# Performance work log

Measured on AMD Instinct MI355X. Metric: run time of the kernel, lower is better.

## Reference

```python
import jax, jax.numpy as jnp
import numpy as np

EMBED_LEN = 512
NUM_FEA = 8   # M
NUM_CLS = 14  # C
BETA = 0.3
BATCH = 8192


def setup_inputs() -> dict:
    key = jax.random.key(0)
    k1, k2, k3 = jax.random.split(key, 3)
    x = jax.random.normal(k1, (BATCH, EMBED_LEN * NUM_FEA), dtype=jnp.float32)
    wordvec_array = jax.random.normal(k2, (1, EMBED_LEN, NUM_CLS), dtype=jnp.float32)
    y = jax.random.randint(k3, (BATCH, NUM_CLS), 0, 2, dtype=jnp.int32)
    # guarantee at least one positive and one negative label per sample
    y = y.at[:, 0].set(1).at[:, -1].set(0)
    return {"x": x, "y": y, "wordvec_array": wordvec_array}


def reference(x, y, wordvec_array):
    B = x.shape[0]
    un = x.reshape(B, EMBED_LEN, -1)            # [B, E, M]
    w = wordvec_array[0]                         # [E, C]
    # dot_prod_all[b, c] = max_m <un[b,:,m], w[:,c]>
    dot = jnp.einsum('bem,ec->bmc', un, w).max(axis=1)   # [B, C]

    P = (y == 1).astype(x.dtype)                 # positive mask [B, C]
    N = 1.0 - P                                  # negative mask [B, C]
    npos = P.sum(axis=-1)                        # [B]
    nneg = N.sum(axis=-1)                        # [B]

    # pairwise v[b,p,n] = dot_neg - dot_pos; sum softplus over masked pairs
    V = dot[:, None, :] - dot[:, :, None]        # [B, C(pos), C(neg)]
    pair_sum = jnp.einsum('bp,bn,bpn->b', P, N, jax.nn.softplus(V))
    # edge case: no negatives -> v = -dot_pos
    noneg_sum = jnp.sum(P * jax.nn.softplus(-dot), axis=-1)
    S = jnp.where(nneg > 0, pair_sum, noneg_sum)
    base = S / npos                              # [B]

    # diversity: unbiased variance of positive-class word vectors over class dim
    mean_w = jnp.einsum('bc,ec->be', P, w) / npos[:, None]          # [B, E]
    ss = jnp.einsum('bc,bec->be', P, (w[None] - mean_w[:, :, None]) ** 2)
    var_w = ss / jnp.maximum(npos - 1.0, 1.0)[:, None]
    var_w = jnp.where((npos == 1.0)[:, None], 0.0, var_w)           # sig = 0 if single positive
    total_var = var_w.sum(axis=-1)               # [B]

    # var_regularization: unbiased var over M, L1 over embed dim
    sig2 = jnp.var(un, axis=2, ddof=1)           # [B, E]
    l1_err = jnp.abs(sig2).sum(axis=-1)          # [B]

    # num_fea > 1 branch
    loss = 2.0 * ((1.0 - BETA) * (1.0 + total_var) * base + BETA * l1_err)
    return loss.mean()
```

## Files before the change

kernel.cpp:

```cpp
#include <hip/hip_runtime.h>
#include <math.h>

#define E_LEN 512
#define M_FEA 8
#define C_CLS 14
#define BATCH 8192
#define S_PER_BLOCK 4

template<int CTRL>
__device__ __forceinline__ float dpp_mov_f(float v) {
  return __int_as_float(__builtin_amdgcn_update_dpp(
      0, __float_as_int(v), CTRL, 0xF, 0xF, false));
}
__device__ __forceinline__ float sum16(float v) {
  v += dpp_mov_f<0x128>(v);
  v += dpp_mov_f<0x124>(v);
  v += dpp_mov_f<0x122>(v);
  v += dpp_mov_f<0x121>(v);
  return v;
}
__device__ __forceinline__ float sum4_16(float v) {
  v += dpp_mov_f<0x128>(v);
  v += dpp_mov_f<0x124>(v);
  return v;
}
__device__ __forceinline__ float max8(float v) {
  v = fmaxf(v, dpp_mov_f<0xB1>(v));
  v = fmaxf(v, dpp_mov_f<0x4E>(v));
  v = fmaxf(v, dpp_mov_f<0x141>(v));
  return v;
}
__device__ __forceinline__ float softplus_f(float v) {
  return fmaxf(v, 0.f) + __logf(1.f + __expf(-fabsf(v)));
}

__global__ void MID_LOSS_prep(const float* __restrict__ w,
                              float* __restrict__ wsf,
                              float* __restrict__ out) {
  __shared__ float wc[E_LEN];
  __shared__ float red[16];
  const int tid = threadIdx.x;
  const int c = blockIdx.x;

  for (int i = tid; i < E_LEN; i += 256) wc[i] = w[i * C_CLS + c];
  __syncthreads();

  const int h = (c >= 7) ? 1 : 0;
  const int ci = c - h * 7;
  for (int i = tid; i < E_LEN; i += 256) {
    int pos = (ci < 6) ? (h * 3584 + (ci >> 1) * 1024 + 2 * i + (ci & 1))
                       : (h * 3584 + 3072 + i);
    wsf[pos] = wc[i];
  }

  for (int c2 = 0; c2 < C_CLS; ++c2) {
    float part = 0.f;
    for (int i = tid; i < E_LEN; i += 256) part = fmaf(wc[i], w[i * C_CLS + c2], part);
    part = sum16(part);
    if ((tid & 15) == 0) red[tid >> 4] = part;
    __syncthreads();
    if (tid == 0) {
      float s = 0.f;
      for (int r = 0; r < 16; ++r) s += red[r];
      wsf[7168 + c * C_CLS + c2] = s;
    }
    __syncthreads();
  }
  if (c == 0 && tid == 0) out[0] = 0.f;
}

__global__ __launch_bounds__(256, 3)
void MID_LOSS_main(const float* __restrict__ x, const int* __restrict__ y,
                   const float* __restrict__ wsf, float* __restrict__ out) {
  __shared__ float w_lds[7168];
  __shared__ float G_lds[196];
  __shared__ float P_lds[C_CLS];
  __shared__ float dotc_lds[C_CLS];
  __shared__ float scratch[14 * 264];
  __shared__ float pair_scr[16];
  __shared__ float g_scr[16];
  __shared__ float l1_scr[8];

  const int tid = threadIdx.x;
  const int lane = tid & 63;
  const int wid = tid >> 6;
  const int ch = wid & 1;
  const int eh = wid >> 1;

#pragma unroll
  for (int i = 0; i < 7; ++i) {
    int idx = tid + i * 256;
    ((float4*)w_lds)[idx] = ((const float4*)wsf)[idx];
  }
  if (tid < 196) G_lds[tid] = wsf[7168 + tid];

  float block_loss = 0.f;

  for (int s = 0; s < S_PER_BLOCK; ++s) {
    const int b = blockIdx.x * S_PER_BLOCK + s;
    const float* xrow = x + (size_t)b * (E_LEN * M_FEA);

    __syncthreads();
    if (tid < C_CLS) P_lds[tid] = (y[b * C_CLS + tid] == 1) ? 1.f : 0.f;

    float U[4][8];
#pragma unroll
    for (int j = 0; j < 4; ++j) {
      const int e = eh * 256 + j * 64 + lane;
      *(float4*)&U[j][0] = *(const float4*)(xrow + e * 8);
      *(float4*)&U[j][4] = *(const float4*)(xrow + e * 8 + 4);
    }
    float acc[7][8];
#pragma unroll
    for (int ci = 0; ci < 7; ++ci)
#pragma unroll
      for (int m = 0; m < 8; ++m) acc[ci][m] = 0.f;
    float l1 = 0.f;
    const float* wb = w_lds + ch * 3584;
#pragma unroll
    for (int j = 0; j < 4; ++j) {
      const int e = eh * 256 + j * 64 + lane;
#pragma unroll
      for (int cp = 0; cp < 3; ++cp) {
        const float2 w2 = *(const float2*)(wb + cp * 1024 + 2 * e);
#pragma unroll
        for (int m = 0; m < 8; ++m) {
          acc[2 * cp][m]     = fmaf(U[j][m], w2.x, acc[2 * cp][m]);
          acc[2 * cp + 1][m] = fmaf(U[j][m], w2.y, acc[2 * cp + 1][m]);
        }
      }
      const float w1 = wb[3072 + e];
#pragma unroll
      for (int m = 0; m < 8; ++m) acc[6][m] = fmaf(U[j][m], w1, acc[6][m]);

      if (ch == 0) {
        float s1 = 0.f, s2 = 0.f;
#pragma unroll
        for (int m = 0; m < 8; ++m) {
          s1 += U[j][m];
          s2 = fmaf(U[j][m], U[j][m], s2);
        }
        const float sig = (s2 - s1 * s1 * 0.125f) * (1.f / 7.f);
        l1 += fabsf(sig);
      }
    }
#pragma unroll
    for (int ci = 0; ci < 7; ++ci)
#pragma unroll
      for (int m = 0; m < 8; ++m) acc[ci][m] = sum4_16(acc[ci][m]);
    if ((lane & 15) < 4) {
      const int part = eh * 16 + (lane >> 4) * 4 + (lane & 3);
#pragma unroll
      for (int ci = 0; ci < 7; ++ci) {
        const int c = ch * 7 + ci;
        *(float4*)(scratch + c * 264 + part * 8) =
            make_float4(acc[ci][0], acc[ci][1], acc[ci][2], acc[ci][3]);
        *(float4*)(scratch + c * 264 + part * 8 + 4) =
            make_float4(acc[ci][4], acc[ci][5], acc[ci][6], acc[ci][7]);
      }
    }
    if (ch == 0) {
      const float l1s = sum16(l1);
      if ((lane & 15) == 0) l1_scr[eh * 4 + (lane >> 4)] = l1s;
    }
    __syncthreads();

    if (wid < 2) {
      const int craw = tid >> 3;
      const int c = (craw > 13) ? 13 : craw;
      const int m = tid & 7;
      float dv = 0.f;
#pragma unroll
      for (int p = 0; p < 32; ++p) dv += scratch[c * 264 + p * 8 + m];
      dv = max8(dv);
      if ((tid & 7) == 0 && craw < 14) dotc_lds[c] = dv;
    }
    __syncthreads();

    {
      const int tt = (tid < 196) ? tid : 0;
      const int p = tt / 14;
      const int n = tt - p * 14;
      const float act = (tid < 196) ? 1.f : 0.f;
      const float Pp = P_lds[p];
      const float Pn = P_lds[n];
      const float v = dotc_lds[n] - dotc_lds[p];
      float aP = act * Pp * (1.f - Pn) * softplus_f(v);
      float aG = act * Pp * Pn * G_lds[tt];
      aP = sum16(aP);
      aG = sum16(aG);
      if ((lane & 15) == 0) {
        pair_scr[tid >> 4] = aP;
        g_scr[tid >> 4] = aG;
      }
    }
    __syncthreads();

    if (tid == 0) {
      float S = 0.f, sumG = 0.f;
#pragma unroll
      for (int r = 0; r < 16; ++r) { S += pair_scr[r]; sumG += g_scr[r]; }
      float l1e = 0.f;
#pragma unroll
      for (int r = 0; r < 8; ++r) l1e += l1_scr[r];
      float npos = 0.f;
      for (int c = 0; c < C_CLS; ++c) npos += P_lds[c];
      const float nneg = (float)C_CLS - npos;
      float base;
      if (nneg > 0.f) {
        base = S / npos;
      } else {
        float t = 0.f;
        for (int c = 0; c < C_CLS; ++c)
          if (P_lds[c] > 0.5f) t += softplus_f(-dotc_lds[c]);
        base = t / npos;
      }
      float sumW2 = 0.f;
      for (int c = 0; c < C_CLS; ++c) sumW2 += P_lds[c] * G_lds[c * C_CLS + c];
      float tv = 0.f;
      if (npos > 1.5f) tv = (sumW2 - sumG / npos) / (npos - 1.f);
      block_loss += 1.4f * (1.f + tv) * base + 0.6f * l1e;
    }
  }
  if (tid == 0) atomicAdd(out, block_loss * (1.f / (float)BATCH));
}

extern "C" void kernel_launch(void* const* d_in, const int* in_sizes, int n_in,
                              void* d_out, int out_size, void* d_ws, size_t ws_size,
                              hipStream_t stream) {
  const float* x = (const float*)d_in[0];
  const int* y = (const int*)d_in[1];
  const float* w = (const float*)d_in[2];
  float* out = (float*)d_out;
  float* wsf = (float*)d_ws;

  MID_LOSS_prep<<<C_CLS, 256, 0, stream>>>(w, wsf, out);
  MID_LOSS_main<<<BATCH / S_PER_BLOCK, 256, 0, stream>>>(x, y, wsf, out);
}
```

Baseline: 218.4 us.

## Split work across M halves, spread atomics over slots, add final reduction

The main kernel now splits waves by feature half instead of class half, so each thread loads only four features and accumulates all 14 classes, with the variance partials exchanged through LDS. The weight permutation moves from the prep kernel into each main block's load phase. The single global atomic is replaced by 256 slot atomics plus a small finishing kernel. Prep collapses to one block computing the Gram matrix. The aims are less per-thread register pressure, less atomic contention and a balanced L1-variance workload. The cost is an extra kernel launch and per-block index math during the weight load.

```diff
diff --git a/kernel.cpp b/kernel.cpp
--- a/kernel.cpp
+++ b/kernel.cpp
@@ -2,10 +2,10 @@
 #include <math.h>
 
 #define E_LEN 512
-#define M_FEA 8
 #define C_CLS 14
 #define BATCH 8192
 #define S_PER_BLOCK 4
+#define NSLOTS 256
 
 template<int CTRL>
 __device__ __forceinline__ float dpp_mov_f(float v) {
@@ -35,145 +35,144 @@
 }
 
 __global__ void MID_LOSS_prep(const float* __restrict__ w,
-                              float* __restrict__ wsf,
-                              float* __restrict__ out) {
-  __shared__ float wc[E_LEN];
-  __shared__ float red[16];
+                              float* __restrict__ wsf) {
+  __shared__ float wl[E_LEN * C_CLS];
   const int tid = threadIdx.x;
-  const int c = blockIdx.x;
-
-  for (int i = tid; i < E_LEN; i += 256) wc[i] = w[i * C_CLS + c];
+#pragma unroll
+  for (int i = 0; i < 7; ++i)
+    ((float4*)wl)[tid + i * 256] = ((const float4*)w)[tid + i * 256];
+  wsf[tid] = 0.f;
   __syncthreads();
-
-  const int h = (c >= 7) ? 1 : 0;
-  const int ci = c - h * 7;
-  for (int i = tid; i < E_LEN; i += 256) {
-    int pos = (ci < 6) ? (h * 3584 + (ci >> 1) * 1024 + 2 * i + (ci & 1))
-                       : (h * 3584 + 3072 + i);
-    wsf[pos] = wc[i];
+  if (tid < 196) {
+    const int p = tid / 14, n = tid - p * 14;
+    float g = 0.f;
+    for (int e = 0; e < E_LEN; ++e)
+      g = fmaf(wl[e * 14 + p], wl[e * 14 + n], g);
+    wsf[NSLOTS + tid] = g;
   }
-
-  for (int c2 = 0; c2 < C_CLS; ++c2) {
-    float part = 0.f;
-    for (int i = tid; i < E_LEN; i += 256) part = fmaf(wc[i], w[i * C_CLS + c2], part);
-    part = sum16(part);
-    if ((tid & 15) == 0) red[tid >> 4] = part;
-    __syncthreads();
-    if (tid == 0) {
-      float s = 0.f;
-      for (int r = 0; r < 16; ++r) s += red[r];
-      wsf[7168 + c * C_CLS + c2] = s;
-    }
-    __syncthreads();
-  }
-  if (c == 0 && tid == 0) out[0] = 0.f;
 }
 
 __global__ __launch_bounds__(256, 3)
 void MID_LOSS_main(const float* __restrict__ x, const int* __restrict__ y,
-                   const float* __restrict__ wsf, float* __restrict__ out) {
-  __shared__ float w_lds[7168];
-  __shared__ float G_lds[196];
-  __shared__ float P_lds[C_CLS];
-  __shared__ float dotc_lds[C_CLS];
-  __shared__ float scratch[14 * 264];
-  __shared__ float pair_scr[16];
-  __shared__ float g_scr[16];
-  __shared__ float l1_scr[8];
+                   const float* __restrict__ w, const float* __restrict__ wsf,
+                   float* __restrict__ slots) {
+  __shared__ float wp_s[7 * 1024];
+  __shared__ float scr[14 * 264];
+  __shared__ float var_s[E_LEN * 2];
+  __shared__ float G_s[196];
+  __shared__ float P_s[C_CLS];
+  __shared__ float dot_s[C_CLS];
+  __shared__ float pair_scr[16], g_scr[16], l1_scr[8];
 
   const int tid = threadIdx.x;
   const int lane = tid & 63;
   const int wid = tid >> 6;
-  const int ch = wid & 1;
+  const int mh = wid & 1;
   const int eh = wid >> 1;
 
 #pragma unroll
   for (int i = 0; i < 7; ++i) {
-    int idx = tid + i * 256;
-    ((float4*)w_lds)[idx] = ((const float4*)wsf)[idx];
+    const int idx = tid + i * 256;
+    const float4 v = ((const float4*)w)[idx];
+    const float vv[4] = {v.x, v.y, v.z, v.w};
+#pragma unroll
+    for (int k = 0; k < 4; ++k) {
+      const int f = idx * 4 + k;
+      const int e = f / 14;
+      const int c = f - e * 14;
+      wp_s[(c >> 1) * 1024 + e * 2 + (c & 1)] = vv[k];
+    }
   }
-  if (tid < 196) G_lds[tid] = wsf[7168 + tid];
+  if (tid < 196) G_s[tid] = wsf[NSLOTS + tid];
 
   float block_loss = 0.f;
 
   for (int s = 0; s < S_PER_BLOCK; ++s) {
     const int b = blockIdx.x * S_PER_BLOCK + s;
-    const float* xrow = x + (size_t)b * (E_LEN * M_FEA);
-
-    __syncthreads();
-    if (tid < C_CLS) P_lds[tid] = (y[b * C_CLS + tid] == 1) ? 1.f : 0.f;
-
-    float U[4][8];
+    const float* xrow = x + (size_t)b * (E_LEN * 8);
+
+    __syncthreads();
+    if (tid < C_CLS) P_s[tid] = (y[b * C_CLS + tid] == 1) ? 1.f : 0.f;
+
+    float U[4][4];
 #pragma unroll
     for (int j = 0; j < 4; ++j) {
       const int e = eh * 256 + j * 64 + lane;
-      *(float4*)&U[j][0] = *(const float4*)(xrow + e * 8);
-      *(float4*)&U[j][4] = *(const float4*)(xrow + e * 8 + 4);
-    }
-    float acc[7][8];
-#pragma unroll
-    for (int ci = 0; ci < 7; ++ci)
-#pragma unroll
-      for (int m = 0; m < 8; ++m) acc[ci][m] = 0.f;
-    float l1 = 0.f;
-    const float* wb = w_lds + ch * 3584;
+      *(float4*)U[j] = *(const float4*)(xrow + e * 8 + mh * 4);
+    }
+    float vs1[4], vs2[4];
+#pragma unroll
+    for (int j = 0; j < 4; ++j) {
+      float s1 = U[j][0] + U[j][1] + U[j][2] + U[j][3];
+      float s2 = U[j][0] * U[j][0];
+      s2 = fmaf(U[j][1], U[j][1], s2);
+      s2 = fmaf(U[j][2], U[j][2], s2);
+      s2 = fmaf(U[j][3], U[j][3], s2);
+      vs1[j] = s1;
+      vs2[j] = s2;
+    }
+    if (mh == 1) {
+#pragma unroll
+      for (int j = 0; j < 4; ++j) {
+        const int e = eh * 256 + j * 64 + lane;
+        *(float2*)(var_s + e * 2) = make_float2(vs1[j], vs2[j]);
+      }
+    }
+    float acc[14][4];
+#pragma unroll
+    for (int c = 0; c < 14; ++c)
+#pragma unroll
+      for (int m = 0; m < 4; ++m) acc[c][m] = 0.f;
 #pragma unroll
     for (int j = 0; j < 4; ++j) {
       const int e = eh * 256 + j * 64 + lane;
-#pragma unroll
-      for (int cp = 0; cp < 3; ++cp) {
-        const float2 w2 = *(const float2*)(wb + cp * 1024 + 2 * e);
-#pragma unroll
-        for (int m = 0; m < 8; ++m) {
+      const float* wb = wp_s + e * 2;
+#pragma unroll
+      for (int cp = 0; cp < 7; ++cp) {
+        const float2 w2 = *(const float2*)(wb + cp * 1024);
+#pragma unroll
+        for (int m = 0; m < 4; ++m) {
           acc[2 * cp][m]     = fmaf(U[j][m], w2.x, acc[2 * cp][m]);
           acc[2 * cp + 1][m] = fmaf(U[j][m], w2.y, acc[2 * cp + 1][m]);
         }
       }
-      const float w1 = wb[3072 + e];
-#pragma unroll
-      for (int m = 0; m < 8; ++m) acc[6][m] = fmaf(U[j][m], w1, acc[6][m]);
-
-      if (ch == 0) {
-        float s1 = 0.f, s2 = 0.f;
-#pragma unroll
-        for (int m = 0; m < 8; ++m) {
-          s1 += U[j][m];
-          s2 = fmaf(U[j][m], U[j][m], s2);
-        }
+    }
+#pragma unroll
+    for (int c = 0; c < 14; ++c)
+#pragma unroll
+      for (int m = 0; m < 4; ++m) acc[c][m] = sum4_16(acc[c][m]);
+    if ((lane & 15) < 4) {
+      const int part = eh * 16 + (lane >> 4) * 4 + (lane & 3);
+#pragma unroll
+      for (int c = 0; c < 14; ++c)
+        *(float4*)(scr + c * 264 + part * 8 + mh * 4) =
+            make_float4(acc[c][0], acc[c][1], acc[c][2], acc[c][3]);
+    }
+    __syncthreads();
+
+    if (mh == 1) {
+      const int r = eh * 64 + lane;
+      const int craw = r >> 3;
+      const int c = (craw > 13) ? 13 : craw;
+      const int m = r & 7;
+      float dv = 0.f;
+#pragma unroll
+      for (int p = 0; p < 32; ++p) dv += scr[c * 264 + p * 8 + m];
+      dv = max8(dv);
+      if ((r & 7) == 0 && craw < 14) dot_s[c] = dv;
+    } else {
+      float l1 = 0.f;
+#pragma unroll
+      for (int j = 0; j < 4; ++j) {
+        const int e = eh * 256 + j * 64 + lane;
+        const float2 o = *(const float2*)(var_s + e * 2);
+        const float s1 = vs1[j] + o.x;
+        const float s2 = vs2[j] + o.y;
         const float sig = (s2 - s1 * s1 * 0.125f) * (1.f / 7.f);
         l1 += fabsf(sig);
       }
-    }
-#pragma unroll
-    for (int ci = 0; ci < 7; ++ci)
-#pragma unroll
-      for (int m = 0; m < 8; ++m) acc[ci][m] = sum4_16(acc[ci][m]);
-    if ((lane & 15) < 4) {
-      const int part = eh * 16 + (lane >> 4) * 4 + (lane & 3);
-#pragma unroll
-      for (int ci = 0; ci < 7; ++ci) {
-        const int c = ch * 7 + ci;
-        *(float4*)(scratch + c * 264 + part * 8) =
-            make_float4(acc[ci][0], acc[ci][1], acc[ci][2], acc[ci][3]);
-        *(float4*)(scratch + c * 264 + part * 8 + 4) =
-            make_float4(acc[ci][4], acc[ci][5], acc[ci][6], acc[ci][7]);
-      }
-    }
-    if (ch == 0) {
-      const float l1s = sum16(l1);
-      if ((lane & 15) == 0) l1_scr[eh * 4 + (lane >> 4)] = l1s;
-    }
-    __syncthreads();
-
-    if (wid < 2) {
-      const int craw = tid >> 3;
-      const int c = (craw > 13) ? 13 : craw;
-      const int m = tid & 7;
-      float dv = 0.f;
-#pragma unroll
-      for (int p = 0; p < 32; ++p) dv += scratch[c * 264 + p * 8 + m];
-      dv = max8(dv);
-      if ((tid & 7) == 0 && craw < 14) dotc_lds[c] = dv;
+      l1 = sum16(l1);
+      if ((lane & 15) == 0) l1_scr[eh * 4 + (lane >> 4)] = l1;
     }
     __syncthreads();
 
@@ -182,11 +181,11 @@
       const int p = tt / 14;
       const int n = tt - p * 14;
       const float act = (tid < 196) ? 1.f : 0.f;
-      const float Pp = P_lds[p];
-      const float Pn = P_lds[n];
-      const float v = dotc_lds[n] - dotc_lds[p];
+      const float Pp = P_s[p];
+      const float Pn = P_s[n];
+      const float v = dot_s[n] - dot_s[p];
       float aP = act * Pp * (1.f - Pn) * softplus_f(v);
-      float aG = act * Pp * Pn * G_lds[tt];
+      float aG = act * Pp * Pn * G_s[tt];
       aP = sum16(aP);
       aG = sum16(aG);
       if ((lane & 15) == 0) {
@@ -199,30 +198,41 @@
     if (tid == 0) {
       float S = 0.f, sumG = 0.f;
 #pragma unroll
-      for (int r = 0; r < 16; ++r) { S += pair_scr[r]; sumG += g_scr[r]; }
+      for (int r2 = 0; r2 < 16; ++r2) { S += pair_scr[r2]; sumG += g_scr[r2]; }
       float l1e = 0.f;
 #pragma unroll
-      for (int r = 0; r < 8; ++r) l1e += l1_scr[r];
+      for (int r2 = 0; r2 < 8; ++r2) l1e += l1_scr[r2];
       float npos = 0.f;
-      for (int c = 0; c < C_CLS; ++c) npos += P_lds[c];
-      const float nneg = (float)C_CLS - npos;
+      for (int c = 0; c < 14; ++c) npos += P_s[c];
+      const float nneg = 14.f - npos;
       float base;
       if (nneg > 0.f) {
         base = S / npos;
       } else {
-        float t = 0.f;
-        for (int c = 0; c < C_CLS; ++c)
-          if (P_lds[c] > 0.5f) t += softplus_f(-dotc_lds[c]);
-        base = t / npos;
+        float t2 = 0.f;
+        for (int c = 0; c < 14; ++c)
+          if (P_s[c] > 0.5f) t2 += softplus_f(-dot_s[c]);
+        base = t2 / npos;
       }
       float sumW2 = 0.f;
-      for (int c = 0; c < C_CLS; ++c) sumW2 += P_lds[c] * G_lds[c * C_CLS + c];
+      for (int c = 0; c < 14; ++c) sumW2 += P_s[c] * G_s[c * 14 + c];
       float tv = 0.f;
       if (npos > 1.5f) tv = (sumW2 - sumG / npos) / (npos - 1.f);
       block_loss += 1.4f * (1.f + tv) * base + 0.6f * l1e;
     }
   }
-  if (tid == 0) atomicAdd(out, block_loss * (1.f / (float)BATCH));
+  if (tid == 0) atomicAdd(&slots[blockIdx.x & (NSLOTS - 1)], block_loss);
+}
+
+__global__ void MID_LOSS_fin(const float* __restrict__ wsf,
+                             float* __restrict__ out) {
+  __shared__ float r[4];
+  const int tid = threadIdx.x;
+  float s = wsf[tid] + wsf[tid + 64] + wsf[tid + 128] + wsf[tid + 192];
+  s = sum16(s);
+  if ((tid & 15) == 0) r[tid >> 4] = s;
+  __syncthreads();
+  if (tid == 0) out[0] = (r[0] + r[1] + r[2] + r[3]) * (1.f / (float)BATCH);
 }
 
 extern "C" void kernel_launch(void* const* d_in, const int* in_sizes, int n_in,
@@ -234,6 +244,7 @@
   float* out = (float*)d_out;
   float* wsf = (float*)d_ws;
 
-  MID_LOSS_prep<<<C_CLS, 256, 0, stream>>>(w, wsf, out);
-  MID_LOSS_main<<<BATCH / S_PER_BLOCK, 256, 0, stream>>>(x, y, wsf, out);
-}
+  MID_LOSS_prep<<<1, 256, 0, stream>>>(w, wsf);
+  MID_LOSS_main<<<BATCH / S_PER_BLOCK, 256, 0, stream>>>(x, y, w, wsf, wsf);
+  MID_LOSS_fin<<<1, 64, 0, stream>>>(wsf, out);
+}
```

After: 212.4 us. 1.03x faster.
